# Optimization experiments

Measured on AMD Instinct MI355X. Metric: run time of the kernel, lower is better.

The kernel has to match this reference:

```python
import jax, jax.numpy as jnp
import numpy as np

N_HEADS = 16

def _rel_emb(table, len_q, len_k):
    # table: [2P+1, d] -> [len_q, len_k, d] via clipped relative distance lookup
    P = (table.shape[0] - 1) // 2
    rel = jnp.arange(len_k)[None, :] - jnp.arange(len_q)[:, None]
    idx = jnp.clip(rel, -P, P) + P
    return table[idx]

def setup_inputs() -> dict:
    key = jax.random.key(0)
    ks = jax.random.split(key, 13)
    B, S, E = 2, 2048, 1024
    P = 128
    d = E // N_HEADS
    s = 0.02
    return {
        "q": jax.random.normal(ks[0], (B, S, E), jnp.float32),
        "k": jax.random.normal(ks[1], (B, S, E), jnp.float32),
        "v": jax.random.normal(ks[2], (B, S, E), jnp.float32),
        "Wq": jax.random.normal(ks[3], (E, E), jnp.float32) * s,
        "bq": jnp.zeros((E,), jnp.float32),
        "Wk": jax.random.normal(ks[4], (E, E), jnp.float32) * s,
        "bk": jnp.zeros((E,), jnp.float32),
        "Wv": jax.random.normal(ks[5], (E, E), jnp.float32) * s,
        "bv": jnp.zeros((E,), jnp.float32),
        "Wo": jax.random.normal(ks[6], (E, E), jnp.float32) * s,
        "bo": jnp.zeros((E,), jnp.float32),
        "rk_table": jax.random.normal(ks[7], (2 * P + 1, d), jnp.float32) * s,
        "rv_table": jax.random.normal(ks[8], (2 * P + 1, d), jnp.float32) * s,
    }

def reference(q, k, v, Wq, bq, Wk, bk, Wv, bv, Wo, bo, rk_table, rv_table):
    B, Sq, E = q.shape
    Sk = k.shape[1]
    H = N_HEADS
    d = E // H
    scale = jnp.sqrt(jnp.asarray(d, q.dtype))

    qh = (q @ Wq.T + bq).reshape(B, Sq, H, d).transpose(0, 2, 1, 3)  # [B,H,Sq,d]
    kh = (k @ Wk.T + bk).reshape(B, Sk, H, d).transpose(0, 2, 1, 3)
    vh = (v @ Wv.T + bv).reshape(B, Sk, H, d).transpose(0, 2, 1, 3)

    qk = jnp.einsum('bhqd,bhkd->bhqk', qh, kh)
    r_k = _rel_emb(rk_table, Sq, Sk)                 # [Sq,Sk,d]
    q_rk = jnp.einsum('bhqd,qkd->bhqk', qh, r_k)
    attn = jax.nn.softmax((qk + q_rk) / scale, axis=-1)  # dropout p=0

    w1 = jnp.einsum('bhqk,bhkd->bhqd', attn, vh)
    r_v = _rel_emb(rv_table, Sq, Sk)
    w2 = jnp.einsum('bhqk,qkd->bhqd', attn, r_v)

    out = (w1 + w2).transpose(0, 2, 1, 3).reshape(B, Sq, E)
    return out @ Wo.T + bo
```

## Files before the change

### kernel.cpp

```cpp
#include <hip/hip_runtime.h>
#include <hip/hip_bf16.h>
#include <cstdint>
#include <cstddef>

#define NH   16
#define DH   64
#define SQ   2048
#define NB   2
#define EM   1024
#define NREL 257
#define QSTR 258
#define SCL  0.18033688f

typedef unsigned short ushort_t;
using bf16x8 = __attribute__((ext_vector_type(8))) __bf16;
using f32x4  = __attribute__((ext_vector_type(4))) float;
#define MFMA16(a, b, c) __builtin_amdgcn_mfma_f32_16x16x32_bf16(a, b, c, 0, 0, 0)

__device__ __forceinline__ ushort_t f2bf(float f) {
    union { float f; unsigned u; } x; x.f = f;
    unsigned r = x.u + 0x7FFFu + ((x.u >> 16) & 1u);
    return (ushort_t)(r >> 16);
}
__device__ __forceinline__ float bf2f(ushort_t u) {
    union { unsigned u; float f; } x; x.u = ((unsigned)u) << 16;
    return x.f;
}
__device__ __forceinline__ int kperm(int x) {
    return (x & ~63) | ((x & 15) << 2) | ((x >> 4) & 3);
}

__global__ __launch_bounds__(256)
void cvt3(const float* __restrict__ a, const float* __restrict__ b,
          const float* __restrict__ c, ushort_t* __restrict__ oa,
          ushort_t* __restrict__ ob, ushort_t* __restrict__ oc, int n)
{
    const float* in = blockIdx.y == 0 ? a : (blockIdx.y == 1 ? b : c);
    ushort_t* out   = blockIdx.y == 0 ? oa : (blockIdx.y == 1 ? ob : oc);
    int i = (blockIdx.x * 256 + threadIdx.x) * 8;
    if (i < n) {
        float4 v0 = *reinterpret_cast<const float4*>(in + i);
        float4 v1 = *reinterpret_cast<const float4*>(in + i + 4);
        union { ushort_t u[8]; uint4 v; } o;
        o.u[0]=f2bf(v0.x); o.u[1]=f2bf(v0.y); o.u[2]=f2bf(v0.z); o.u[3]=f2bf(v0.w);
        o.u[4]=f2bf(v1.x); o.u[5]=f2bf(v1.y); o.u[6]=f2bf(v1.z); o.u[7]=f2bf(v1.w);
        *reinterpret_cast<uint4*>(out + i) = o.v;
    }
}
__global__ __launch_bounds__(256)
void cvt4(const float* __restrict__ a, const float* __restrict__ b,
          const float* __restrict__ c, const float* __restrict__ d,
          ushort_t* __restrict__ oa, ushort_t* __restrict__ ob,
          ushort_t* __restrict__ oc, ushort_t* __restrict__ od, int n)
{
    const float* in = blockIdx.y == 0 ? a : (blockIdx.y == 1 ? b :
                      (blockIdx.y == 2 ? c : d));
    ushort_t* out   = blockIdx.y == 0 ? oa : (blockIdx.y == 1 ? ob :
                      (blockIdx.y == 2 ? oc : od));
    int i = (blockIdx.x * 256 + threadIdx.x) * 8;
    if (i < n) {
        float4 v0 = *reinterpret_cast<const float4*>(in + i);
        float4 v1 = *reinterpret_cast<const float4*>(in + i + 4);
        union { ushort_t u[8]; uint4 v; } o;
        o.u[0]=f2bf(v0.x); o.u[1]=f2bf(v0.y); o.u[2]=f2bf(v0.z); o.u[3]=f2bf(v0.w);
        o.u[4]=f2bf(v1.x); o.u[5]=f2bf(v1.y); o.u[6]=f2bf(v1.z); o.u[7]=f2bf(v1.w);
        *reinterpret_cast<uint4*>(out + i) = o.v;
    }
}

__global__ __launch_bounds__(256)
void prep_tables(const float* __restrict__ rv, const float* __restrict__ rk,
                 ushort_t* __restrict__ rvT, ushort_t* __restrict__ rkb)
{
    int idx = blockIdx.x * 256 + threadIdx.x;
    if (idx < 64 * 256) {
        int d = idx >> 8, c = idx & 255;
        rvT[d * 256 + kperm(c)] = f2bf(rv[(size_t)(c + 1) * DH + d]);
    }
    idx -= 64 * 256;
    if (idx >= 0 && idx < 272 * 64) {
        int j = idx >> 6, d2 = idx & 63;
        rkb[idx] = (j < NREL) ? f2bf(rk[(size_t)j * DH + d2]) : (ushort_t)0;
    }
}

template<int MODE>
__global__ __launch_bounds__(256)
void gemm_bt(const ushort_t* __restrict__ A, const ushort_t* __restrict__ W,
             const float* __restrict__ bias, void* __restrict__ dstv,
             int M, int N, int K)
{
    __shared__ ushort_t As[128 * 40];
    __shared__ ushort_t Bs[128 * 40];
    const int t = threadIdx.x, lane = t & 63;
    const int wv = t >> 6, wr = wv >> 1, wc = wv & 1;
    const int g = lane >> 4, c16 = lane & 15;

    const int nwg = gridDim.x * gridDim.y;
    int flat = blockIdx.y * gridDim.x + blockIdx.x;
    int rm = (flat & 7) * (nwg >> 3) + (flat >> 3);
    const int n0 = (rm % gridDim.x) * 128;
    const int m0 = (rm / gridDim.x) * 128;

    f32x4 acc[4][4];
#pragma unroll
    for (int i = 0; i < 4; ++i)
#pragma unroll
        for (int j = 0; j < 4; ++j) acc[i][j] = (f32x4){0.f, 0.f, 0.f, 0.f};

    for (int k0 = 0; k0 < K; k0 += 32) {
        __syncthreads();
#pragma unroll
        for (int l = 0; l < 2; ++l) {
            const int fid = t + 256 * l;
            const int row = fid >> 2, ch = fid & 3;
            uint4 av = *reinterpret_cast<const uint4*>(A + (size_t)(m0 + row) * K + k0 + ch * 8);
            uint4 wv4 = *reinterpret_cast<const uint4*>(W + (size_t)(n0 + row) * K + k0 + ch * 8);
            *reinterpret_cast<uint4*>(As + row * 40 + ch * 8) = av;
            *reinterpret_cast<uint4*>(Bs + row * 40 + ch * 8) = wv4;
        }
        __syncthreads();

        bf16x8 af[4], bfr[4];
#pragma unroll
        for (int i = 0; i < 4; ++i)
            af[i] = *reinterpret_cast<const bf16x8*>(As + (wr * 64 + i * 16 + c16) * 40 + g * 8);
#pragma unroll
        for (int j = 0; j < 4; ++j)
            bfr[j] = *reinterpret_cast<const bf16x8*>(Bs + (wc * 64 + j * 16 + c16) * 40 + g * 8);
#pragma unroll
        for (int i = 0; i < 4; ++i)
#pragma unroll
            for (int j = 0; j < 4; ++j)
                acc[i][j] = MFMA16(af[i], bfr[j], acc[i][j]);
    }

#pragma unroll
    for (int j = 0; j < 4; ++j) {
        const int n = n0 + wc * 64 + j * 16 + c16;
        const float bn = bias[n];
#pragma unroll
        for (int i = 0; i < 4; ++i) {
#pragma unroll
            for (int r = 0; r < 4; ++r) {
                const int m = m0 + wr * 64 + i * 16 + 4 * g + r;
                const float vv = acc[i][j][r] + bn;
                if (MODE == 0) {
                    ((float*)dstv)[(size_t)m * N + n] = vv;
                } else {
                    const int b = m >> 11, s = m & (SQ - 1);
                    const int h = n >> 6, dd = n & 63;
                    if (MODE == 1) {
                        ((ushort_t*)dstv)[(((size_t)b * NH + h) * SQ + s) * DH + dd] = f2bf(vv);
                    } else {
                        const int sp = kperm(s);
                        ((ushort_t*)dstv)[(((size_t)b * NH + h) * DH + dd) * SQ + sp] = f2bf(vv);
                    }
                }
            }
        }
    }
}

__global__ __launch_bounds__(256)
void qrel_mfma(const ushort_t* __restrict__ qh, const ushort_t* __restrict__ rkb,
               ushort_t* __restrict__ qrel)
{
    const int t = threadIdx.x, lane = t & 63, w = t >> 6;
    const int g = lane >> 4, c16 = lane & 15;
    const size_t r0 = (size_t)blockIdx.x * 64 + w * 16;

    bf16x8 af[2];
#pragma unroll
    for (int ks = 0; ks < 2; ++ks)
        af[ks] = *reinterpret_cast<const bf16x8*>(qh + (r0 + c16) * DH + ks * 32 + g * 8);

    f32x4 acc[17];
#pragma unroll
    for (int n = 0; n < 17; ++n) acc[n] = (f32x4){0.f, 0.f, 0.f, 0.f};
#pragma unroll
    for (int n = 0; n < 17; ++n)
#pragma unroll
        for (int ks = 0; ks < 2; ++ks) {
            bf16x8 bf = *reinterpret_cast<const bf16x8*>(
                rkb + (size_t)(16 * n + c16) * DH + ks * 32 + g * 8);
            acc[n] = MFMA16(af[ks], bf, acc[n]);
        }
#pragma unroll
    for (int n = 0; n < 17; ++n) {
        const int j = 16 * n + c16;
        if (j < NREL) {
#pragma unroll
            for (int r = 0; r < 4; ++r)
                qrel[(r0 + 4 * g + r) * QSTR + j] = f2bf(acc[n][r] * SCL);
        }
    }
}

__global__ __launch_bounds__(256, 4)
void attn_flash(const ushort_t* __restrict__ qh, const ushort_t* __restrict__ kh,
                const ushort_t* __restrict__ vt, const ushort_t* __restrict__ qrel,
                ushort_t* __restrict__ Pg, float* __restrict__ w1g,
                float* __restrict__ lacg, float* __restrict__ b0g)
{
    __shared__ ushort_t Ks[64 * 72];
    __shared__ ushort_t Vs[64 * 72];
    __shared__ ushort_t PQs[64 * 72];

    const int t = threadIdx.x, lane = t & 63, w = t >> 6;
    const int g = lane >> 4, c16 = lane & 15;
    const int nwg = gridDim.x * gridDim.y;
    int flat = blockIdx.y * gridDim.x + blockIdx.x;
    int rmid = (flat & 7) * (nwg >> 3) + (flat >> 3);
    const int q0 = (rmid & 31) * 64;
    const int bh = rmid >> 5;

#pragma unroll
    for (int l = 0; l < 2; ++l) {
        const int fid = t + 256 * l;
        const int row = fid >> 3, ch = fid & 7;
        uint4 v = *reinterpret_cast<const uint4*>(
            qh + ((size_t)bh * SQ + q0 + row) * DH + ch * 8);
        *reinterpret_cast<uint4*>(PQs + row * 72 + ch * 8) = v;
    }
    __syncthreads();
    bf16x8 qf[2];
#pragma unroll
    for (int ks = 0; ks < 2; ++ks)
        qf[ks] = *reinterpret_cast<const bf16x8*>(PQs + (w * 16 + c16) * 72 + ks * 32 + g * 8);

    float q0add[4], q256add[4];
#pragma unroll
    for (int i = 0; i < 4; ++i) {
        const size_t r = (size_t)bh * SQ + q0 + w * 16 + 4 * g + i;
        q0add[i]   = bf2f(qrel[r * QSTR + 0]);
        q256add[i] = bf2f(qrel[r * QSTR + 256]);
    }

    f32x4 w1[4];
#pragma unroll
    for (int n = 0; n < 4; ++n) w1[n] = (f32x4){0.f, 0.f, 0.f, 0.f};
    float lac[4] = {0.f,0.f,0.f,0.f}, b0[4] = {0.f,0.f,0.f,0.f}, b256[4] = {0.f,0.f,0.f,0.f};

    const int row_l = t >> 3, ch_l = t & 7;
    const int row_h = row_l + 32;
    uint4 kr0, kr1, vr0, vr1;
    {
        kr0 = *reinterpret_cast<const uint4*>(kh + ((size_t)bh * SQ + row_l) * DH + ch_l * 8);
        kr1 = *reinterpret_cast<const uint4*>(kh + ((size_t)bh * SQ + row_h) * DH + ch_l * 8);
        vr0 = *reinterpret_cast<const uint4*>(vt + ((size_t)bh * DH + row_l) * SQ + ch_l * 8);
        vr1 = *reinterpret_cast<const uint4*>(vt + ((size_t)bh * DH + row_h) * SQ + ch_l * 8);
    }

    for (int k0 = 0; k0 < SQ; k0 += 64) {
        __syncthreads();
        *reinterpret_cast<uint4*>(Ks + row_l * 72 + ch_l * 8) = kr0;
        *reinterpret_cast<uint4*>(Ks + row_h * 72 + ch_l * 8) = kr1;
        *reinterpret_cast<uint4*>(Vs + row_l * 72 + ch_l * 8) = vr0;
        *reinterpret_cast<uint4*>(Vs + row_h * 72 + ch_l * 8) = vr1;
        __syncthreads();
        if (k0 + 64 < SQ) {
            kr0 = *reinterpret_cast<const uint4*>(kh + ((size_t)bh * SQ + k0 + 64 + row_l) * DH + ch_l * 8);
            kr1 = *reinterpret_cast<const uint4*>(kh + ((size_t)bh * SQ + k0 + 64 + row_h) * DH + ch_l * 8);
            vr0 = *reinterpret_cast<const uint4*>(vt + ((size_t)bh * DH + row_l) * SQ + k0 + 64 + ch_l * 8);
            vr1 = *reinterpret_cast<const uint4*>(vt + ((size_t)bh * DH + row_h) * SQ + k0 + 64 + ch_l * 8);
        }

        f32x4 s[4];
#pragma unroll
        for (int n = 0; n < 4; ++n) s[n] = (f32x4){0.f, 0.f, 0.f, 0.f};
        __builtin_amdgcn_s_setprio(1);
#pragma unroll
        for (int ks = 0; ks < 2; ++ks)
#pragma unroll
            for (int n = 0; n < 4; ++n) {
                bf16x8 kf = *reinterpret_cast<const bf16x8*>(
                    Ks + (16 * n + c16) * 72 + ks * 32 + g * 8);
                s[n] = MFMA16(qf[ks], kf, s[n]);
            }
        __builtin_amdgcn_s_setprio(0);

        const int rel0 = k0 - q0;
        float rsum[4] = {0.f, 0.f, 0.f, 0.f};
        if (rel0 <= -192 || rel0 >= 192) {
            const bool lo = rel0 < 0;
#pragma unroll
            for (int i = 0; i < 4; ++i) {
                const float add = lo ? q0add[i] : q256add[i];
#pragma unroll
                for (int n = 0; n < 4; ++n) {
                    const float p = exp2f(fmaf(s[n][i], SCL, add));
                    s[n][i] = p; rsum[i] += p;
                }
                if (lo) b0[i] += rsum[i]; else b256[i] += rsum[i];
            }
        } else {
#pragma unroll
            for (int i = 0; i < 4; ++i) {
                const int qloc = w * 16 + 4 * g + i;
                const int qg = q0 + qloc;
                const ushort_t* qrow = qrel + ((size_t)bh * SQ + qg) * QSTR;
#pragma unroll
                for (int n = 0; n < 4; ++n) {
                    const int rel = (k0 + 16 * n + c16) - qg;
                    const int idx = rel < -128 ? 0 : (rel > 128 ? 256 : rel + 128);
                    const float add = bf2f(qrow[idx]);
                    const float p = exp2f(fmaf(s[n][i], SCL, add));
                    s[n][i] = p; rsum[i] += p;
                    if (rel <= -128)      b0[i] += p;
                    else if (rel >= 128)  b256[i] += p;
                    else {
                        const int x = rel + 127;
                        const int col = (x & 192) | ((x & 15) << 2) | ((x >> 4) & 3);
                        Pg[((size_t)bh * SQ + qg) * 256 + col] = f2bf(p);
                    }
                }
            }
        }
#pragma unroll
        for (int i = 0; i < 4; ++i) lac[i] += rsum[i];

#pragma unroll
        for (int i = 0; i < 4; ++i) {
            unsigned lop = (unsigned)f2bf(s[0][i]) | ((unsigned)f2bf(s[1][i]) << 16);
            unsigned hip = (unsigned)f2bf(s[2][i]) | ((unsigned)f2bf(s[3][i]) << 16);
            *reinterpret_cast<uint2*>(PQs + (w * 16 + 4 * g + i) * 72 + c16 * 4) =
                make_uint2(lop, hip);
        }
        __builtin_amdgcn_s_setprio(1);
#pragma unroll
        for (int ks = 0; ks < 2; ++ks) {
            bf16x8 pf = *reinterpret_cast<const bf16x8*>(
                PQs + (w * 16 + c16) * 72 + ks * 32 + g * 8);
#pragma unroll
            for (int n = 0; n < 4; ++n) {
                bf16x8 vf = *reinterpret_cast<const bf16x8*>(
                    Vs + (16 * n + c16) * 72 + ks * 32 + g * 8);
                w1[n] = MFMA16(pf, vf, w1[n]);
            }
        }
        __builtin_amdgcn_s_setprio(0);
    }

#pragma unroll
    for (int m = 1; m < 16; m <<= 1)
#pragma unroll
        for (int i = 0; i < 4; ++i) {
            lac[i]  += __shfl_xor(lac[i],  m, 64);
            b0[i]   += __shfl_xor(b0[i],   m, 64);
            b256[i] += __shfl_xor(b256[i], m, 64);
        }
    if (c16 == 0) {
#pragma unroll
        for (int i = 0; i < 4; ++i) {
            const size_t row = (size_t)bh * SQ + q0 + w * 16 + 4 * g + i;
            lacg[row] = lac[i]; b0g[row] = b0[i];
            Pg[row * 256 + 255] = f2bf(b256[i]);
        }
    }
#pragma unroll
    for (int n = 0; n < 4; ++n)
#pragma unroll
        for (int i = 0; i < 4; ++i) {
            const size_t row = (size_t)bh * SQ + q0 + w * 16 + 4 * g + i;
            w1g[row * DH + 16 * n + c16] = w1[n][i];
        }
}

__global__ __launch_bounds__(256)
void band_gemm(const ushort_t* __restrict__ Pg, const ushort_t* __restrict__ rvT,
               const float* __restrict__ rv_f32, const float* __restrict__ w1g,
               const float* __restrict__ lacg, const float* __restrict__ b0g,
               ushort_t* __restrict__ wout)
{
    __shared__ ushort_t Pb[64 * 264];
    const int t = threadIdx.x, lane = t & 63, w = t >> 6;
    const int g = lane >> 4, c16 = lane & 15;
    const size_t r0 = (size_t)blockIdx.x * 64;

#pragma unroll
    for (int l = 0; l < 8; ++l) {
        const int fid = t + 256 * l;
        const int row = fid >> 5, ch = fid & 31;
        uint4 v = *reinterpret_cast<const uint4*>(Pg + (r0 + row) * 256 + ch * 8);
        *reinterpret_cast<uint4*>(Pb + row * 264 + ch * 8) = v;
    }
    __syncthreads();

    f32x4 acc[4];
#pragma unroll
    for (int n = 0; n < 4; ++n) acc[n] = (f32x4){0.f, 0.f, 0.f, 0.f};
#pragma unroll
    for (int ks = 0; ks < 8; ++ks) {
        bf16x8 pm = *reinterpret_cast<const bf16x8*>(
            Pb + (w * 16 + c16) * 264 + ks * 32 + g * 8);
#pragma unroll
        for (int n = 0; n < 4; ++n) {
            bf16x8 rf = *reinterpret_cast<const bf16x8*>(
                rvT + (size_t)(16 * n + c16) * 256 + ks * 32 + g * 8);
            acc[n] = MFMA16(pm, rf, acc[n]);
        }
    }

#pragma unroll
    for (int i = 0; i < 4; ++i) {
        const size_t row = r0 + w * 16 + 4 * g + i;
        const float inv = 1.0f / lacg[row];
        const float vb0 = b0g[row];
        const int b = (int)(row >> 15), h = (int)((row >> 11) & 15), s = (int)(row & 2047);
#pragma unroll
        for (int n = 0; n < 4; ++n) {
            const int col = 16 * n + c16;
            const float val = (w1g[row * DH + col] + acc[n][i] + vb0 * rv_f32[col]) * inv;
            wout[(((size_t)b * SQ + s) * NH + h) * DH + col] = f2bf(val);
        }
    }
}

extern "C" void kernel_launch(void* const* d_in, const int* in_sizes, int n_in,
                              void* d_out, int out_size, void* d_ws, size_t ws_size,
                              hipStream_t stream)
{
    const float* q  = (const float*)d_in[0];
    const float* k  = (const float*)d_in[1];
    const float* v  = (const float*)d_in[2];
    const float* Wq = (const float*)d_in[3];
    const float* bq = (const float*)d_in[4];
    const float* Wk = (const float*)d_in[5];
    const float* bk = (const float*)d_in[6];
    const float* Wv = (const float*)d_in[7];
    const float* bv = (const float*)d_in[8];
    const float* Wo = (const float*)d_in[9];
    const float* bo = (const float*)d_in[10];
    const float* rk = (const float*)d_in[11];
    const float* rv = (const float*)d_in[12];

    char* ws = (char*)d_ws;
    auto alloc = [&](size_t bytes) { char* p = ws; ws += bytes; return p; };
    const size_t QB = (size_t)NB * SQ * EM * 2;
    const size_t WB = (size_t)EM * EM * 2;
    const size_t NR = (size_t)NB * NH * SQ;

    char* region0 = alloc(NR * 256 * 2);
    ushort_t* Pg  = (ushort_t*)region0;
    ushort_t* qbf = (ushort_t*)region0;
    ushort_t* kbf = (ushort_t*)(region0 + QB);
    ushort_t* vbf = (ushort_t*)(region0 + 2 * QB);
    ushort_t* Wqb = (ushort_t*)(region0 + 3 * QB);
    ushort_t* Wkb = (ushort_t*)(region0 + 3 * QB + WB);
    ushort_t* Wvb = (ushort_t*)(region0 + 3 * QB + 2 * WB);

    ushort_t* Wob  = (ushort_t*)alloc(WB);
    ushort_t* qhb  = (ushort_t*)alloc(QB);
    ushort_t* khb  = (ushort_t*)alloc(QB);
    ushort_t* vtb  = (ushort_t*)alloc(QB);
    ushort_t* wbuf = (ushort_t*)alloc(QB);
    ushort_t* rvT  = (ushort_t*)alloc(64 * 256 * 2);
    ushort_t* rkb  = (ushort_t*)alloc(272 * 64 * 2);
    ushort_t* qrel = (ushort_t*)alloc(NR * QSTR * 2);
    float*    w1g  = (float*)alloc(NR * DH * 4);
    float*    lacg = (float*)alloc(NR * 4);
    float*    b0g  = (float*)alloc(NR * 4);

    const int NQ = NB * SQ * EM;
    const int NW = EM * EM;
    cvt3<<<dim3(NQ / 2048, 3), 256, 0, stream>>>(q, k, v, qbf, kbf, vbf, NQ);
    cvt4<<<dim3(NW / 2048, 4), 256, 0, stream>>>(Wq, Wk, Wv, Wo, Wqb, Wkb, Wvb, Wob, NW);
    prep_tables<<<132, 256, 0, stream>>>(rv, rk, rvT, rkb);

    const int M = NB * SQ;
    dim3 gg(EM / 128, M / 128);
    gemm_bt<1><<<gg, 256, 0, stream>>>(qbf, Wqb, bq, qhb, M, EM, EM);
    gemm_bt<1><<<gg, 256, 0, stream>>>(kbf, Wkb, bk, khb, M, EM, EM);
    gemm_bt<2><<<gg, 256, 0, stream>>>(vbf, Wvb, bv, vtb, M, EM, EM);
    qrel_mfma<<<(int)(NR / 64), 256, 0, stream>>>(qhb, rkb, qrel);

    hipMemsetAsync(Pg, 0, NR * 256 * 2, stream);

    attn_flash<<<dim3(32, 32), 256, 0, stream>>>(qhb, khb, vtb, qrel,
                                                 Pg, w1g, lacg, b0g);
    band_gemm<<<(int)(NR / 64), 256, 0, stream>>>(Pg, rvT, rv, w1g, lacg, b0g, wbuf);
    gemm_bt<0><<<gg, 256, 0, stream>>>(wbuf, Wob, bo, d_out, M, EM, EM);
}
```

Measured before the change: 319.8 us.

## Write band probabilities as coalesced tiles and drop the memset of the band buffer

attn_flash previously scattered individual bf16 probabilities into a permuted 256-column band buffer that had to be zeroed by a large memset first. It now writes the five diagonal-band 64x64 P tiles contiguously as packed 4-element stores, and stores b256 in its own array. band_gemm gathers those tiles into a zeroed shared-memory band with the permuted layout. The change also switches to hardware bf16 conversion with a vector pack helper. The goal is to remove the memset and the uncoalesced 2-byte global scatter, at the cost of a slightly larger tile buffer and extra shared-memory scatter work in band_gemm.

```diff
diff --git a/kernel.cpp b/kernel.cpp
--- a/kernel.cpp
+++ b/kernel.cpp
@@ -14,17 +14,21 @@
 
 typedef unsigned short ushort_t;
 using bf16x8 = __attribute__((ext_vector_type(8))) __bf16;
+using bf16x4 = __attribute__((ext_vector_type(4))) __bf16;
 using f32x4  = __attribute__((ext_vector_type(4))) float;
 #define MFMA16(a, b, c) __builtin_amdgcn_mfma_f32_16x16x32_bf16(a, b, c, 0, 0, 0)
 
 __device__ __forceinline__ ushort_t f2bf(float f) {
-    union { float f; unsigned u; } x; x.f = f;
-    unsigned r = x.u + 0x7FFFu + ((x.u >> 16) & 1u);
-    return (ushort_t)(r >> 16);
+    union { __bf16 h; ushort_t u; } x; x.h = (__bf16)f; return x.u;
 }
 __device__ __forceinline__ float bf2f(ushort_t u) {
     union { unsigned u; float f; } x; x.u = ((unsigned)u) << 16;
     return x.f;
+}
+__device__ __forceinline__ uint2 pack4(float a, float b, float c, float d) {
+    union { bf16x4 v; uint2 u; } x;
+    x.v = (bf16x4){ (__bf16)a, (__bf16)b, (__bf16)c, (__bf16)d };
+    return x.u;
 }
 __device__ __forceinline__ int kperm(int x) {
     return (x & ~63) | ((x & 15) << 2) | ((x >> 4) & 3);
@@ -41,10 +45,9 @@
     if (i < n) {
         float4 v0 = *reinterpret_cast<const float4*>(in + i);
         float4 v1 = *reinterpret_cast<const float4*>(in + i + 4);
-        union { ushort_t u[8]; uint4 v; } o;
-        o.u[0]=f2bf(v0.x); o.u[1]=f2bf(v0.y); o.u[2]=f2bf(v0.z); o.u[3]=f2bf(v0.w);
-        o.u[4]=f2bf(v1.x); o.u[5]=f2bf(v1.y); o.u[6]=f2bf(v1.z); o.u[7]=f2bf(v1.w);
-        *reinterpret_cast<uint4*>(out + i) = o.v;
+        uint2 lo = pack4(v0.x, v0.y, v0.z, v0.w);
+        uint2 hi = pack4(v1.x, v1.y, v1.z, v1.w);
+        *reinterpret_cast<uint4*>(out + i) = make_uint4(lo.x, lo.y, hi.x, hi.y);
     }
 }
 __global__ __launch_bounds__(256)
@@ -61,10 +64,9 @@
     if (i < n) {
         float4 v0 = *reinterpret_cast<const float4*>(in + i);
         float4 v1 = *reinterpret_cast<const float4*>(in + i + 4);
-        union { ushort_t u[8]; uint4 v; } o;
-        o.u[0]=f2bf(v0.x); o.u[1]=f2bf(v0.y); o.u[2]=f2bf(v0.z); o.u[3]=f2bf(v0.w);
-        o.u[4]=f2bf(v1.x); o.u[5]=f2bf(v1.y); o.u[6]=f2bf(v1.z); o.u[7]=f2bf(v1.w);
-        *reinterpret_cast<uint4*>(out + i) = o.v;
+        uint2 lo = pack4(v0.x, v0.y, v0.z, v0.w);
+        uint2 hi = pack4(v1.x, v1.y, v1.z, v1.w);
+        *reinterpret_cast<uint4*>(out + i) = make_uint4(lo.x, lo.y, hi.x, hi.y);
     }
 }
 
@@ -200,8 +202,9 @@
 __global__ __launch_bounds__(256, 4)
 void attn_flash(const ushort_t* __restrict__ qh, const ushort_t* __restrict__ kh,
                 const ushort_t* __restrict__ vt, const ushort_t* __restrict__ qrel,
-                ushort_t* __restrict__ Pg, float* __restrict__ w1g,
-                float* __restrict__ lacg, float* __restrict__ b0g)
+                ushort_t* __restrict__ Ptile, float* __restrict__ w1g,
+                float* __restrict__ lacg, float* __restrict__ b0g,
+                float* __restrict__ b256g)
 {
     __shared__ ushort_t Ks[64 * 72];
     __shared__ ushort_t Vs[64 * 72];
@@ -214,6 +217,7 @@
     int rmid = (flat & 7) * (nwg >> 3) + (flat >> 3);
     const int q0 = (rmid & 31) * 64;
     const int bh = rmid >> 5;
+    const size_t Gbase = ((size_t)bh * 32 + (q0 >> 6)) * 5;
 
 #pragma unroll
     for (int l = 0; l < 2; ++l) {
@@ -293,40 +297,56 @@
                     s[n][i] = p; rsum[i] += p;
                 }
                 if (lo) b0[i] += rsum[i]; else b256[i] += rsum[i];
+                *reinterpret_cast<uint2*>(PQs + (w * 16 + 4 * g + i) * 72 + c16 * 4) =
+                    pack4(s[0][i], s[1][i], s[2][i], s[3][i]);
             }
-        } else {
+        } else if (rel0 == -128 || rel0 == 128) {
+            const int tix = (rel0 >> 6) + 2;
 #pragma unroll
             for (int i = 0; i < 4; ++i) {
                 const int qloc = w * 16 + 4 * g + i;
                 const int qg = q0 + qloc;
                 const ushort_t* qrow = qrel + ((size_t)bh * SQ + qg) * QSTR;
+                float z[4];
 #pragma unroll
                 for (int n = 0; n < 4; ++n) {
                     const int rel = (k0 + 16 * n + c16) - qg;
                     const int idx = rel < -128 ? 0 : (rel > 128 ? 256 : rel + 128);
-                    const float add = bf2f(qrow[idx]);
-                    const float p = exp2f(fmaf(s[n][i], SCL, add));
+                    const float p = exp2f(fmaf(s[n][i], SCL, bf2f(qrow[idx])));
                     s[n][i] = p; rsum[i] += p;
+                    const bool inb = (rel >= -127) & (rel <= 127);
+                    z[n] = inb ? p : 0.f;
                     if (rel <= -128)      b0[i] += p;
                     else if (rel >= 128)  b256[i] += p;
-                    else {
-                        const int x = rel + 127;
-                        const int col = (x & 192) | ((x & 15) << 2) | ((x >> 4) & 3);
-                        Pg[((size_t)bh * SQ + qg) * 256 + col] = f2bf(p);
-                    }
                 }
+                *reinterpret_cast<uint2*>(PQs + qloc * 72 + c16 * 4) =
+                    pack4(s[0][i], s[1][i], s[2][i], s[3][i]);
+                *reinterpret_cast<uint2*>(
+                    Ptile + ((Gbase + tix) * 64 + qloc) * 64 + 4 * c16) =
+                    pack4(z[0], z[1], z[2], z[3]);
             }
+        } else {
+            const int tix = (rel0 >> 6) + 2;
+#pragma unroll
+            for (int i = 0; i < 4; ++i) {
+                const int qloc = w * 16 + 4 * g + i;
+                const int qg = q0 + qloc;
+                const ushort_t* qrow = qrel + ((size_t)bh * SQ + qg) * QSTR;
+#pragma unroll
+                for (int n = 0; n < 4; ++n) {
+                    const int rel = (k0 + 16 * n + c16) - qg;
+                    const float p = exp2f(fmaf(s[n][i], SCL, bf2f(qrow[rel + 128])));
+                    s[n][i] = p; rsum[i] += p;
+                }
+                const uint2 pk = pack4(s[0][i], s[1][i], s[2][i], s[3][i]);
+                *reinterpret_cast<uint2*>(PQs + qloc * 72 + c16 * 4) = pk;
+                *reinterpret_cast<uint2*>(
+                    Ptile + ((Gbase + tix) * 64 + qloc) * 64 + 4 * c16) = pk;
+            }
         }
 #pragma unroll
         for (int i = 0; i < 4; ++i) lac[i] += rsum[i];
 
-#pragma unroll
-        for (int i = 0; i < 4; ++i) {
-            unsigned lop = (unsigned)f2bf(s[0][i]) | ((unsigned)f2bf(s[1][i]) << 16);
-            unsigned hip = (unsigned)f2bf(s[2][i]) | ((unsigned)f2bf(s[3][i]) << 16);
-            *reinterpret_cast<uint2*>(PQs + (w * 16 + 4 * g + i) * 72 + c16 * 4) =
-                make_uint2(lop, hip);
-        }
         __builtin_amdgcn_s_setprio(1);
 #pragma unroll
         for (int ks = 0; ks < 2; ++ks) {
@@ -354,8 +374,7 @@
 #pragma unroll
         for (int i = 0; i < 4; ++i) {
             const size_t row = (size_t)bh * SQ + q0 + w * 16 + 4 * g + i;
-            lacg[row] = lac[i]; b0g[row] = b0[i];
-            Pg[row * 256 + 255] = f2bf(b256[i]);
+            lacg[row] = lac[i]; b0g[row] = b0[i]; b256g[row] = b256[i];
         }
     }
 #pragma unroll
@@ -368,23 +387,40 @@
 }
 
 __global__ __launch_bounds__(256)
-void band_gemm(const ushort_t* __restrict__ Pg, const ushort_t* __restrict__ rvT,
+void band_gemm(const ushort_t* __restrict__ Ptile, const ushort_t* __restrict__ rvT,
                const float* __restrict__ rv_f32, const float* __restrict__ w1g,
                const float* __restrict__ lacg, const float* __restrict__ b0g,
-               ushort_t* __restrict__ wout)
-{
-    __shared__ ushort_t Pb[64 * 264];
+               const float* __restrict__ b256g, ushort_t* __restrict__ wout)
+{
+    __shared__ ushort_t Pband[64 * 264];
     const int t = threadIdx.x, lane = t & 63, w = t >> 6;
     const int g = lane >> 4, c16 = lane & 15;
-    const size_t r0 = (size_t)blockIdx.x * 64;
-
-#pragma unroll
-    for (int l = 0; l < 8; ++l) {
-        const int fid = t + 256 * l;
-        const int row = fid >> 5, ch = fid & 31;
-        uint4 v = *reinterpret_cast<const uint4*>(Pg + (r0 + row) * 256 + ch * 8);
-        *reinterpret_cast<uint4*>(Pb + row * 264 + ch * 8) = v;
-    }
+    const int G = blockIdx.x;
+    const size_t r0 = (size_t)G * 64;
+    const int q0 = (G & 31) * 64;
+
+    for (int i = t; i < 64 * 264 / 2; i += 256)
+        reinterpret_cast<unsigned*>(Pband)[i] = 0u;
+    __syncthreads();
+
+    for (int u = t; u < 5 * 64 * 16; u += 256) {
+        const int tix = u >> 10;
+        const int kt0 = q0 + (tix - 2) * 64;
+        if (kt0 < 0 || kt0 >= SQ) continue;
+        const int qloc = (u >> 4) & 63;
+        const int c = u & 15;
+        uint2 pv = *reinterpret_cast<const uint2*>(
+            Ptile + (((size_t)G * 5 + tix) * 64 + qloc) * 64 + 4 * c);
+        const ushort_t* pe = reinterpret_cast<const ushort_t*>(&pv);
+        const int relbase = (tix - 2) * 64 - qloc + 127;
+#pragma unroll
+        for (int n = 0; n < 4; ++n) {
+            const int x = relbase + 16 * n + c;
+            if (x >= 0 && x <= 254)
+                Pband[qloc * 264 + ((x & ~63) | ((x & 15) << 2) | ((x >> 4) & 3))] = pe[n];
+        }
+    }
+    if (t < 64) Pband[t * 264 + 255] = f2bf(b256g[r0 + t]);
     __syncthreads();
 
     f32x4 acc[4];
@@ -393,7 +429,7 @@
 #pragma unroll
     for (int ks = 0; ks < 8; ++ks) {
         bf16x8 pm = *reinterpret_cast<const bf16x8*>(
-            Pb + (w * 16 + c16) * 264 + ks * 32 + g * 8);
+            Pband + (w * 16 + c16) * 264 + ks * 32 + g * 8);
 #pragma unroll
         for (int n = 0; n < 4; ++n) {
             bf16x8 rf = *reinterpret_cast<const bf16x8*>(
@@ -441,8 +477,8 @@
     const size_t WB = (size_t)EM * EM * 2;
     const size_t NR = (size_t)NB * NH * SQ;
 
-    char* region0 = alloc(NR * 256 * 2);
-    ushort_t* Pg  = (ushort_t*)region0;
+    char* region0 = alloc(NR * 320 * 2);
+    ushort_t* Ptile = (ushort_t*)region0;
     ushort_t* qbf = (ushort_t*)region0;
     ushort_t* kbf = (ushort_t*)(region0 + QB);
     ushort_t* vbf = (ushort_t*)(region0 + 2 * QB);
@@ -461,6 +497,7 @@
     float*    w1g  = (float*)alloc(NR * DH * 4);
     float*    lacg = (float*)alloc(NR * 4);
     float*    b0g  = (float*)alloc(NR * 4);
+    float*    b256g= (float*)alloc(NR * 4);
 
     const int NQ = NB * SQ * EM;
     const int NW = EM * EM;
@@ -475,10 +512,9 @@
     gemm_bt<2><<<gg, 256, 0, stream>>>(vbf, Wvb, bv, vtb, M, EM, EM);
     qrel_mfma<<<(int)(NR / 64), 256, 0, stream>>>(qhb, rkb, qrel);
 
-    hipMemsetAsync(Pg, 0, NR * 256 * 2, stream);
-
     attn_flash<<<dim3(32, 32), 256, 0, stream>>>(qhb, khb, vtb, qrel,
-                                                 Pg, w1g, lacg, b0g);
-    band_gemm<<<(int)(NR / 64), 256, 0, stream>>>(Pg, rvT, rv, w1g, lacg, b0g, wbuf);
+                                                 Ptile, w1g, lacg, b0g, b256g);
+    band_gemm<<<(int)(NR / 64), 256, 0, stream>>>(Ptile, rvT, rv, w1g, lacg,
+                                                  b0g, b256g, wbuf);
     gemm_bt<0><<<gg, 256, 0, stream>>>(wbuf, Wob, bo, d_out, M, EM, EM);
 }
```

Result: faster. 279.8 us (-12.5%).
